# Optimization experiments

Measured on AMD Instinct MI355X. Metric: run time of the kernel, lower is better.

Reference implementation:

```python
import jax, jax.numpy as jnp
import numpy as np

N_SAMPLES = 128
AGENTS = 64
D = 128          # latent_size
EDIM = 2         # edge attr dim
N = N_SAMPLES * AGENTS
EPS = 1e-5


def _build_edges():
    a = np.arange(AGENTS)
    rows = np.repeat(a, AGENTS)
    cols = np.tile(a, AGENTS)
    mask = rows != cols  # fully connected, no self loops
    rows, cols = rows[mask], cols[mask]
    offsets = (np.arange(N_SAMPLES) * AGENTS)[:, None]
    src = (rows[None, :] + offsets).ravel().astype(np.int32)  # edge_index[0]
    dst = (cols[None, :] + offsets).ravel().astype(np.int32)  # edge_index[1]
    return src, dst


def setup_inputs() -> dict:
    key = jax.random.key(0)
    ks = jax.random.split(key, 16)
    src, dst = _build_edges()
    zin = 2 * D + EDIM  # CGConv concat [x_i, x_j, e]
    inp = {
        "gnn_in": jax.random.normal(ks[0], (N, D), jnp.float32),
        "centers": jax.random.normal(ks[1], (N, EDIM), jnp.float32),
        "edge_src": jnp.asarray(src),
        "edge_dst": jnp.asarray(dst),
    }
    for li, base in ((1, 2), (2, 8)):
        inp[f"Wf{li}"] = jax.random.normal(ks[base + 0], (zin, D), jnp.float32) / np.sqrt(zin)
        inp[f"bf{li}"] = jnp.zeros((D,), jnp.float32)
        inp[f"Ws{li}"] = jax.random.normal(ks[base + 1], (zin, D), jnp.float32) / np.sqrt(zin)
        inp[f"bs{li}"] = jnp.zeros((D,), jnp.float32)
        inp[f"gamma{li}"] = jnp.ones((D,), jnp.float32)
        inp[f"beta{li}"] = jnp.zeros((D,), jnp.float32)
    return inp


def _cgconv(x, e, src, dst, Wf, bf, Ws, bs, gamma, beta):
    # message: z = [x_i(target), x_j(source), e]; sigmoid(Wf z) * softplus(Ws z)
    z = jnp.concatenate([x[dst], x[src], e], axis=-1)  # [E, 2D+2]
    m = jax.nn.sigmoid(z @ Wf + bf) * jax.nn.softplus(z @ Ws + bs)
    agg = jax.ops.segment_sum(m, dst, num_segments=N)  # scatter-add at targets
    # batch norm (training-mode batch stats) then residual, as in PyG CGConv
    mu = agg.mean(axis=0)
    var = agg.var(axis=0)
    agg = (agg - mu) * jax.lax.rsqrt(var + EPS) * gamma + beta
    return agg + x


def reference(gnn_in, centers, edge_src, edge_dst,
              Wf1, bf1, Ws1, bs1, gamma1, beta1,
              Wf2, bf2, Ws2, bs2, gamma2, beta2):
    # edge_attr = centers[col] - centers[row]
    e = centers[edge_dst] - centers[edge_src]  # [E, 2]
    x = jax.nn.relu(_cgconv(gnn_in, e, edge_src, edge_dst, Wf1, bf1, Ws1, bs1, gamma1, beta1))
    x = jax.nn.relu(_cgconv(x, e, edge_src, edge_dst, Wf2, bf2, Ws2, bs2, gamma2, beta2))
    return x
```

## Files before the change

### kernel.cpp

```cpp
#include <hip/hip_runtime.h>
#include <hip/hip_bf16.h>

#define NSAMP 128
#define AGENTS 64
#define D 128
#define NN (NSAMP * AGENTS)
#define LOG2E 1.44269504088896340736f
#define LN2   0.69314718055994530942f
#define EPSF  1e-5f

typedef __attribute__((ext_vector_type(8))) short short8;
typedef __attribute__((ext_vector_type(4))) float floatx4;

__device__ __forceinline__ float u2f(unsigned v) {
    float f; __builtin_memcpy(&f, &v, 4); return f;
}
__device__ __forceinline__ unsigned f2u(float f) {
    unsigned v; __builtin_memcpy(&v, &f, 4); return v;
}
__device__ __forceinline__ unsigned short f2bf(float f) {
    unsigned x; __builtin_memcpy(&x, &f, 4);
    return (unsigned short)((x + 0x7FFFu + ((x >> 16) & 1u)) >> 16);
}

__global__ __launch_bounds__(256) void cvt_kernel(
    const float* __restrict__ Wf1, const float* __restrict__ Ws1,
    const float* __restrict__ Wf2, const float* __restrict__ Ws2,
    unsigned short* __restrict__ WT, float* __restrict__ sacc)
{
    int b = blockIdx.x;
    if (b < 64) {
        int rr = b * 16 + (threadIdx.x >> 4);
        int kk = (threadIdx.x & 15) * 8;
        int layer = rr >> 9, rem = rr & 511, arr = rem >> 7, c = rem & 127;
        const float* M = (arr < 2) ? (layer ? Wf2 : Wf1) : (layer ? Ws2 : Ws1);
        int side = arr & 1;
        short8 s;
        #pragma unroll
        for (int j = 0; j < 8; ++j)
            s[j] = (short)f2bf(M[(size_t)(side * 128 + kk + j) * D + c]);
        *(short8*)&WT[(size_t)(layer * 4 + arr) * 16384 + c * 128 + kk] = s;
    } else {
        sacc[threadIdx.x]       = 0.f;
        sacc[256 + threadIdx.x] = 0.f;
    }
}

__global__ __launch_bounds__(256, 4) void prep_edge(
    const float* __restrict__ xin,
    const unsigned short* __restrict__ WT,
    const float* __restrict__ centers,
    const float* __restrict__ Wf, const float* __restrict__ bf_,
    const float* __restrict__ Ws, const float* __restrict__ bs_,
    float* __restrict__ agg,
    float* __restrict__ sacc)
{
    const int s = blockIdx.x >> 3, q = blockIdx.x & 7;
    const int nbase = s * AGENTS;
    const int tid = threadIdx.x, w = tid >> 6, lane = tid & 63;
    const int quad = lane >> 4, l16 = lane & 15;

    __shared__ unsigned int EApk[64][17];
    __shared__ unsigned int EBpk[64][17];

    const int col = q * 16 + l16;
    short8 a[4];
    {
        const float* xr = xin + (size_t)(nbase + w * 16 + l16) * D + quad * 8;
        #pragma unroll
        for (int kc = 0; kc < 4; ++kc) {
            float4 v0 = *(const float4*)(xr + kc * 32);
            float4 v1 = *(const float4*)(xr + kc * 32 + 4);
            short8 t;
            t[0] = (short)f2bf(v0.x); t[1] = (short)f2bf(v0.y);
            t[2] = (short)f2bf(v0.z); t[3] = (short)f2bf(v0.w);
            t[4] = (short)f2bf(v1.x); t[5] = (short)f2bf(v1.y);
            t[6] = (short)f2bf(v1.z); t[7] = (short)f2bf(v1.w);
            a[kc] = t;
        }
    }
    floatx4 acc[4];
    #pragma unroll
    for (int arr = 0; arr < 4; ++arr) {
        const unsigned short* wp = WT + ((size_t)arr * 128 + col) * 128 + quad * 8;
        floatx4 ac = {0.f, 0.f, 0.f, 0.f};
        #pragma unroll
        for (int kc = 0; kc < 4; ++kc)
            ac = __builtin_amdgcn_mfma_f32_16x16x32_bf16(
                a[kc], *(const short8*)(wp + kc * 32), ac, 0, 0, 0);
        acc[arr] = ac;
    }
    const float cwf0 = Wf[256 * D + col], cwf1 = Wf[257 * D + col];
    const float cws0 = Ws[256 * D + col], cws1 = Ws[257 * D + col];
    const float bfv = bf_[col], bsv = bs_[col];
    #pragma unroll
    for (int r = 0; r < 4; ++r) {
        int row = w * 16 + quad * 4 + r;
        int n = nbase + row;
        float ce0 = centers[2 * n], ce1 = centers[2 * n + 1];
        float ctf = fmaf(ce0, cwf0, ce1 * cwf1);
        float cts = fmaf(ce0, cws0, ce1 * cws1);
        unsigned eaf = (unsigned)f2bf(__builtin_amdgcn_exp2f(-LOG2E * (acc[0][r] + ctf + bfv)));
        unsigned eas = (unsigned)f2bf(__builtin_amdgcn_exp2f( LOG2E * (acc[2][r] + cts + bsv)));
        unsigned ebf = (unsigned)f2bf(__builtin_amdgcn_exp2f(-LOG2E * (acc[1][r] - ctf)));
        unsigned ebs = (unsigned)f2bf(__builtin_amdgcn_exp2f( LOG2E * (acc[3][r] - cts)));
        EApk[row][l16] = eaf | (eas << 16);
        EBpk[row][l16] = ebf | (ebs << 16);
    }
    __syncthreads();

    const int cl = tid & 15, slot = tid >> 4;
    const int c = q * 16 + cl;
    float eaf[4], eas[4], ac2[4];
    #pragma unroll
    for (int i = 0; i < 4; ++i) {
        unsigned pk = EApk[slot * 4 + i][cl];
        eaf[i] = u2f(pk << 16);
        eas[i] = u2f(pk & 0xFFFF0000u);
        ac2[i] = 0.f;
    }
    #pragma unroll 4
    for (int j = 0; j < 64; ++j) {
        unsigned pk = EBpk[j][cl];
        float ebf = u2f(pk << 16);
        float ebs = u2f(pk & 0xFFFF0000u);
        #pragma unroll
        for (int i = 0; i < 4; ++i) {
            float sg = __builtin_amdgcn_rcpf(fmaf(eaf[i], ebf, 1.f));
            float lg = __builtin_amdgcn_logf(fmaf(eas[i], ebs, 1.f));
            ac2[i] = fmaf(sg, lg, ac2[i]);
        }
    }
    float s1 = 0.f, s2 = 0.f;
    #pragma unroll
    for (int i = 0; i < 4; ++i) {
        int d = slot * 4 + i;
        unsigned pk = EBpk[d][cl];
        float ebf = u2f(pk << 16);
        float ebs = u2f(pk & 0xFFFF0000u);
        float sg = __builtin_amdgcn_rcpf(fmaf(eaf[i], ebf, 1.f));
        float lg = __builtin_amdgcn_logf(fmaf(eas[i], ebs, 1.f));
        float v = (ac2[i] - sg * lg) * LN2;
        agg[(size_t)(nbase + d) * D + c] = v;
        s1 += v; s2 += v * v;
    }
    __syncthreads();
    EApk[slot][cl] = f2u(s1);
    EBpk[slot][cl] = f2u(s2);
    __syncthreads();
    #pragma unroll
    for (int off = 8; off >= 1; off >>= 1) {
        if (slot < off) {
            EApk[slot][cl] = f2u(u2f(EApk[slot][cl]) + u2f(EApk[slot + off][cl]));
            EBpk[slot][cl] = f2u(u2f(EBpk[slot][cl]) + u2f(EBpk[slot + off][cl]));
        }
        __syncthreads();
    }
    if (slot == 0) {
        atomicAdd(&sacc[c],       u2f(EApk[0][cl]));
        atomicAdd(&sacc[128 + c], u2f(EBpk[0][cl]));
    }
}

__global__ __launch_bounds__(256) void bn_kernel(
    const float* __restrict__ agg, const float* __restrict__ xin,
    const float* __restrict__ sacc,
    const float* __restrict__ gamma, const float* __restrict__ beta,
    float* __restrict__ outp)
{
    const int t = blockIdx.x * 256 + threadIdx.x;
    const int n = t >> 4;
    const int c = (t & 15) * 8;
    size_t off = (size_t)n * D + c;
    const float inv = 1.f / NN;
    float v[8];
    #pragma unroll
    for (int h = 0; h < 2; ++h) {
        float4 a  = *(const float4*)&agg[off + h * 4];
        float4 xv = *(const float4*)&xin[off + h * 4];
        float4 s1 = *(const float4*)&sacc[c + h * 4];
        float4 s2 = *(const float4*)&sacc[128 + c + h * 4];
        float4 gm = *(const float4*)&gamma[c + h * 4];
        float4 bt = *(const float4*)&beta[c + h * 4];
        float mu, var, rs;
        mu = s1.x * inv; var = s2.x * inv - mu * mu; rs = rsqrtf(var + EPSF);
        v[h*4+0] = fmaxf(0.f, fmaf((a.x - mu) * rs, gm.x, bt.x) + xv.x);
        mu = s1.y * inv; var = s2.y * inv - mu * mu; rs = rsqrtf(var + EPSF);
        v[h*4+1] = fmaxf(0.f, fmaf((a.y - mu) * rs, gm.y, bt.y) + xv.y);
        mu = s1.z * inv; var = s2.z * inv - mu * mu; rs = rsqrtf(var + EPSF);
        v[h*4+2] = fmaxf(0.f, fmaf((a.z - mu) * rs, gm.z, bt.z) + xv.z);
        mu = s1.w * inv; var = s2.w * inv - mu * mu; rs = rsqrtf(var + EPSF);
        v[h*4+3] = fmaxf(0.f, fmaf((a.w - mu) * rs, gm.w, bt.w) + xv.w);
    }
    *(float4*)&outp[off]     = *(float4*)&v[0];
    *(float4*)&outp[off + 4] = *(float4*)&v[4];
}

extern "C" void kernel_launch(void* const* d_in, const int* in_sizes, int n_in,
                              void* d_out, int out_size, void* d_ws, size_t ws_size,
                              hipStream_t stream) {
    const float* x0      = (const float*)d_in[0];
    const float* centers = (const float*)d_in[1];
    const float* Wf[2] = { (const float*)d_in[4],  (const float*)d_in[10] };
    const float* bf[2] = { (const float*)d_in[5],  (const float*)d_in[11] };
    const float* Ws[2] = { (const float*)d_in[6],  (const float*)d_in[12] };
    const float* bs[2] = { (const float*)d_in[7],  (const float*)d_in[13] };
    const float* gm[2] = { (const float*)d_in[8],  (const float*)d_in[14] };
    const float* bt[2] = { (const float*)d_in[9],  (const float*)d_in[15] };

    const size_t ND = (size_t)NN * D;
    unsigned short* ws_u = (unsigned short*)d_ws;
    unsigned short* WT = ws_u;
    float* fbase = (float*)(WT + 2 * 65536);
    float* agg   = fbase;
    float* x1    = fbase + ND;
    float* sacc  = fbase + 2 * ND;

    float* outp = (float*)d_out;

    cvt_kernel<<<dim3(65), dim3(256), 0, stream>>>(
        Wf[0], Ws[0], Wf[1], Ws[1], WT, sacc);

    prep_edge<<<dim3(1024), dim3(256), 0, stream>>>(
        x0, WT, centers, Wf[0], bf[0], Ws[0], bs[0], agg, sacc);
    bn_kernel<<<dim3(512), dim3(256), 0, stream>>>(
        agg, x0, sacc, gm[0], bt[0], x1);

    prep_edge<<<dim3(1024), dim3(256), 0, stream>>>(
        x1, WT + 65536, centers, Wf[1], bf[1], Ws[1], bs[1], agg, sacc + 256);
    bn_kernel<<<dim3(512), dim3(256), 0, stream>>>(
        agg, x1, sacc + 256, gm[1], bt[1], outp);
}
```

Measured before the change: 148.0 us.

## Fuse whole two-layer GNN into one cooperative persistent kernel with grid syncs

Replaces the five separate launches (weight conversion, two edge-message kernels, two batchnorm kernels) with a single cooperative kernel that uses grid-wide syncs between phases. The first batchnorm plus ReLU is folded into the second layer's input loading, so the x1 round trip through memory goes away, and the final output recomputes layer-1 activations from agg1 and x0. The aim is to cut launch overhead and global traffic. In exchange it adds three grid barriers, limits the grid to the number of blocks that fit at once so samples are looped per block, and keeps the old multi-kernel path as a fallback.

Result: slower. 418.4 us (+182.6%).

```diff
diff --git a/kernel.cpp b/kernel.cpp
--- a/kernel.cpp
+++ b/kernel.cpp
@@ -1,5 +1,8 @@
 #include <hip/hip_runtime.h>
 #include <hip/hip_bf16.h>
+#include <hip/hip_cooperative_groups.h>
+
+namespace cg = cooperative_groups;
 
 #define NSAMP 128
 #define AGENTS 64
@@ -21,6 +24,273 @@
 __device__ __forceinline__ unsigned short f2bf(float f) {
     unsigned x; __builtin_memcpy(&x, &f, 4);
     return (unsigned short)((x + 0x7FFFu + ((x >> 16) & 1u)) >> 16);
+}
+
+__device__ __forceinline__ void mfma_gates(
+    const short8 (&a)[4], const unsigned short* __restrict__ wl,
+    const float* __restrict__ Wfp, const float* __restrict__ bfp,
+    const float* __restrict__ Wsp, const float* __restrict__ bsp,
+    const float* __restrict__ centers,
+    int nbase, int w, int quad, int l16, int col,
+    unsigned int (*EApk)[17], unsigned int (*EBpk)[17])
+{
+    floatx4 acc[4];
+    #pragma unroll
+    for (int arr = 0; arr < 4; ++arr) {
+        const unsigned short* wp = wl + ((size_t)arr * 128 + col) * 128 + quad * 8;
+        floatx4 ac = {0.f, 0.f, 0.f, 0.f};
+        #pragma unroll
+        for (int kc = 0; kc < 4; ++kc)
+            ac = __builtin_amdgcn_mfma_f32_16x16x32_bf16(
+                a[kc], *(const short8*)(wp + kc * 32), ac, 0, 0, 0);
+        acc[arr] = ac;
+    }
+    const float cwf0 = Wfp[256 * D + col], cwf1 = Wfp[257 * D + col];
+    const float cws0 = Wsp[256 * D + col], cws1 = Wsp[257 * D + col];
+    const float bfv = bfp[col], bsv = bsp[col];
+    #pragma unroll
+    for (int r = 0; r < 4; ++r) {
+        int row = w * 16 + quad * 4 + r;
+        int n = nbase + row;
+        float ce0 = centers[2 * n], ce1 = centers[2 * n + 1];
+        float ctf = fmaf(ce0, cwf0, ce1 * cwf1);
+        float cts = fmaf(ce0, cws0, ce1 * cws1);
+        unsigned eaf = (unsigned)f2bf(__builtin_amdgcn_exp2f(-LOG2E * (acc[0][r] + ctf + bfv)));
+        unsigned eas = (unsigned)f2bf(__builtin_amdgcn_exp2f( LOG2E * (acc[2][r] + cts + bsv)));
+        unsigned ebf = (unsigned)f2bf(__builtin_amdgcn_exp2f(-LOG2E * (acc[1][r] - ctf)));
+        unsigned ebs = (unsigned)f2bf(__builtin_amdgcn_exp2f( LOG2E * (acc[3][r] - cts)));
+        EApk[row][l16] = eaf | (eas << 16);
+        EBpk[row][l16] = ebf | (ebs << 16);
+    }
+}
+
+__device__ __forceinline__ void phaseB(
+    const unsigned int (*EApk)[17], const unsigned int (*EBpk)[17],
+    int cl, int slot, float (&v)[4], float& s1, float& s2)
+{
+    float eaf[4], eas[4], ac2[4];
+    #pragma unroll
+    for (int i = 0; i < 4; ++i) {
+        unsigned pk = EApk[slot * 4 + i][cl];
+        eaf[i] = u2f(pk << 16);
+        eas[i] = u2f(pk & 0xFFFF0000u);
+        ac2[i] = 0.f;
+    }
+    #pragma unroll 4
+    for (int j = 0; j < 64; ++j) {
+        unsigned pk = EBpk[j][cl];
+        float ebf = u2f(pk << 16);
+        float ebs = u2f(pk & 0xFFFF0000u);
+        #pragma unroll
+        for (int i = 0; i < 4; ++i) {
+            float sg = __builtin_amdgcn_rcpf(fmaf(eaf[i], ebf, 1.f));
+            float lg = __builtin_amdgcn_logf(fmaf(eas[i], ebs, 1.f));
+            ac2[i] = fmaf(sg, lg, ac2[i]);
+        }
+    }
+    s1 = 0.f; s2 = 0.f;
+    #pragma unroll
+    for (int i = 0; i < 4; ++i) {
+        int dd = slot * 4 + i;
+        unsigned pk = EBpk[dd][cl];
+        float ebf = u2f(pk << 16);
+        float ebs = u2f(pk & 0xFFFF0000u);
+        float sg = __builtin_amdgcn_rcpf(fmaf(eaf[i], ebf, 1.f));
+        float lg = __builtin_amdgcn_logf(fmaf(eas[i], ebs, 1.f));
+        v[i] = (ac2[i] - sg * lg) * LN2;
+        s1 += v[i]; s2 += v[i] * v[i];
+    }
+}
+
+__device__ __forceinline__ void stats_tree(
+    unsigned int (*EApk)[17], unsigned int (*EBpk)[17],
+    int cl, int slot, int c, float s1, float s2, float* __restrict__ sc)
+{
+    __syncthreads();
+    EApk[slot][cl] = f2u(s1);
+    EBpk[slot][cl] = f2u(s2);
+    __syncthreads();
+    #pragma unroll
+    for (int off = 8; off >= 1; off >>= 1) {
+        if (slot < off) {
+            EApk[slot][cl] = f2u(u2f(EApk[slot][cl]) + u2f(EApk[slot + off][cl]));
+            EBpk[slot][cl] = f2u(u2f(EBpk[slot][cl]) + u2f(EBpk[slot + off][cl]));
+        }
+        __syncthreads();
+    }
+    if (slot == 0) {
+        atomicAdd(&sc[c],       u2f(EApk[0][cl]));
+        atomicAdd(&sc[128 + c], u2f(EBpk[0][cl]));
+    }
+}
+
+__global__ __launch_bounds__(256, 4) void fused_gnn(
+    const float* __restrict__ x0, const float* __restrict__ centers,
+    const float* __restrict__ Wf1, const float* __restrict__ bf1,
+    const float* __restrict__ Ws1, const float* __restrict__ bs1,
+    const float* __restrict__ gm1, const float* __restrict__ bt1,
+    const float* __restrict__ Wf2, const float* __restrict__ bf2,
+    const float* __restrict__ Ws2, const float* __restrict__ bs2,
+    const float* __restrict__ gm2, const float* __restrict__ bt2,
+    unsigned short* __restrict__ WT, float* __restrict__ agg1,
+    float* __restrict__ agg2, float* __restrict__ sacc,
+    float* __restrict__ outp)
+{
+    cg::grid_group grid = cg::this_grid();
+    const int tid = threadIdx.x, w = tid >> 6, lane = tid & 63;
+    const int quad = lane >> 4, l16 = lane & 15;
+    const int cl = tid & 15, slot = tid >> 4;
+    const int q = blockIdx.x & 7;
+    const int s0 = blockIdx.x >> 3;
+    const int sStep = gridDim.x >> 3;
+    const int c = q * 16 + cl;
+    const int col = q * 16 + l16;
+
+    __shared__ unsigned int EApk[64][17];
+    __shared__ unsigned int EBpk[64][17];
+    __shared__ float bnA[128], bnB[128];
+    __shared__ float bn2A[128], bn2B[128];
+
+    for (int job = blockIdx.x; job < 65; job += gridDim.x) {
+        if (job < 64) {
+            int rr = job * 16 + (tid >> 4);
+            int kk = (tid & 15) * 8;
+            int layer = rr >> 9, rem = rr & 511, arr = rem >> 7, wc = rem & 127;
+            const float* M = (arr < 2) ? (layer ? Wf2 : Wf1) : (layer ? Ws2 : Ws1);
+            int side = arr & 1;
+            short8 sv;
+            #pragma unroll
+            for (int j = 0; j < 8; ++j)
+                sv[j] = (short)f2bf(M[(size_t)(side * 128 + kk + j) * D + wc]);
+            *(short8*)&WT[(size_t)(layer * 4 + arr) * 16384 + wc * 128 + kk] = sv;
+        } else {
+            sacc[tid] = 0.f;
+            sacc[256 + tid] = 0.f;
+        }
+    }
+    __builtin_amdgcn_fence(__ATOMIC_RELEASE, "agent");
+    grid.sync();
+    __builtin_amdgcn_fence(__ATOMIC_ACQUIRE, "agent");
+
+    {
+        float s1T = 0.f, s2T = 0.f;
+        for (int s = s0; s < NSAMP; s += sStep) {
+            const int nbase = s * AGENTS;
+            short8 a[4];
+            const float* xr = x0 + (size_t)(nbase + w * 16 + l16) * D + quad * 8;
+            #pragma unroll
+            for (int kc = 0; kc < 4; ++kc) {
+                float4 v0 = *(const float4*)(xr + kc * 32);
+                float4 v1 = *(const float4*)(xr + kc * 32 + 4);
+                short8 t;
+                t[0] = (short)f2bf(v0.x); t[1] = (short)f2bf(v0.y);
+                t[2] = (short)f2bf(v0.z); t[3] = (short)f2bf(v0.w);
+                t[4] = (short)f2bf(v1.x); t[5] = (short)f2bf(v1.y);
+                t[6] = (short)f2bf(v1.z); t[7] = (short)f2bf(v1.w);
+                a[kc] = t;
+            }
+            mfma_gates(a, WT, Wf1, bf1, Ws1, bs1, centers, nbase, w, quad, l16,
+                       col, EApk, EBpk);
+            __syncthreads();
+            float v1a[4], s1, s2;
+            phaseB(EApk, EBpk, cl, slot, v1a, s1, s2);
+            #pragma unroll
+            for (int i = 0; i < 4; ++i)
+                agg1[(size_t)(nbase + slot * 4 + i) * D + c] = v1a[i];
+            s1T += s1; s2T += s2;
+            __syncthreads();
+        }
+        stats_tree(EApk, EBpk, cl, slot, c, s1T, s2T, sacc);
+    }
+    __builtin_amdgcn_fence(__ATOMIC_RELEASE, "agent");
+    grid.sync();
+    __builtin_amdgcn_fence(__ATOMIC_ACQUIRE, "agent");
+
+    if (tid < 128) {
+        const float inv = 1.f / NN;
+        float mu = sacc[tid] * inv;
+        float var = sacc[128 + tid] * inv - mu * mu;
+        float rs = rsqrtf(var + EPSF);
+        float A = rs * gm1[tid];
+        bnA[tid] = A;
+        bnB[tid] = fmaf(-mu, A, bt1[tid]);
+    }
+    __syncthreads();
+    {
+        float s1T = 0.f, s2T = 0.f;
+        for (int s = s0; s < NSAMP; s += sStep) {
+            const int nbase = s * AGENTS;
+            short8 a[4];
+            const size_t ro = (size_t)(nbase + w * 16 + l16) * D + quad * 8;
+            #pragma unroll
+            for (int kc = 0; kc < 4; ++kc) {
+                int cc = quad * 8 + kc * 32;
+                float4 g0 = *(const float4*)&agg1[ro + kc * 32];
+                float4 g1 = *(const float4*)&agg1[ro + kc * 32 + 4];
+                float4 x0v = *(const float4*)(x0 + ro + kc * 32);
+                float4 x1v = *(const float4*)(x0 + ro + kc * 32 + 4);
+                float4 A0 = *(const float4*)&bnA[cc], A1 = *(const float4*)&bnA[cc + 4];
+                float4 B0 = *(const float4*)&bnB[cc], B1 = *(const float4*)&bnB[cc + 4];
+                short8 t;
+                t[0] = (short)f2bf(fmaxf(0.f, fmaf(g0.x, A0.x, B0.x) + x0v.x));
+                t[1] = (short)f2bf(fmaxf(0.f, fmaf(g0.y, A0.y, B0.y) + x0v.y));
+                t[2] = (short)f2bf(fmaxf(0.f, fmaf(g0.z, A0.z, B0.z) + x0v.z));
+                t[3] = (short)f2bf(fmaxf(0.f, fmaf(g0.w, A0.w, B0.w) + x0v.w));
+                t[4] = (short)f2bf(fmaxf(0.f, fmaf(g1.x, A1.x, B1.x) + x1v.x));
+                t[5] = (short)f2bf(fmaxf(0.f, fmaf(g1.y, A1.y, B1.y) + x1v.y));
+                t[6] = (short)f2bf(fmaxf(0.f, fmaf(g1.z, A1.z, B1.z) + x1v.z));
+                t[7] = (short)f2bf(fmaxf(0.f, fmaf(g1.w, A1.w, B1.w) + x1v.w));
+                a[kc] = t;
+            }
+            mfma_gates(a, WT + 65536, Wf2, bf2, Ws2, bs2, centers, nbase, w,
+                       quad, l16, col, EApk, EBpk);
+            __syncthreads();
+            float v2a[4], s1, s2;
+            phaseB(EApk, EBpk, cl, slot, v2a, s1, s2);
+            #pragma unroll
+            for (int i = 0; i < 4; ++i)
+                agg2[(size_t)(nbase + slot * 4 + i) * D + c] = v2a[i];
+            s1T += s1; s2T += s2;
+            __syncthreads();
+        }
+        stats_tree(EApk, EBpk, cl, slot, c, s1T, s2T, sacc + 256);
+    }
+    __builtin_amdgcn_fence(__ATOMIC_RELEASE, "agent");
+    grid.sync();
+    __builtin_amdgcn_fence(__ATOMIC_ACQUIRE, "agent");
+
+    if (tid < 128) {
+        const float inv = 1.f / NN;
+        float mu = sacc[256 + tid] * inv;
+        float var = sacc[384 + tid] * inv - mu * mu;
+        float rs = rsqrtf(var + EPSF);
+        float A = rs * gm2[tid];
+        bn2A[tid] = A;
+        bn2B[tid] = fmaf(-mu, A, bt2[tid]);
+    }
+    __syncthreads();
+    for (int t = blockIdx.x * 256 + tid; t < NN * 16; t += gridDim.x * 256) {
+        int n = t >> 4, c8 = (t & 15) * 8;
+        size_t off = (size_t)n * D + c8;
+        float o[8];
+        #pragma unroll
+        for (int h = 0; h < 2; ++h) {
+            float4 g2 = *(const float4*)&agg2[off + h * 4];
+            float4 g1 = *(const float4*)&agg1[off + h * 4];
+            float4 xv = *(const float4*)&x0[off + h * 4];
+            int cc = c8 + h * 4;
+            o[h*4+0] = fmaxf(0.f, fmaf(g2.x, bn2A[cc+0], bn2B[cc+0]) +
+                       fmaxf(0.f, fmaf(g1.x, bnA[cc+0], bnB[cc+0]) + xv.x));
+            o[h*4+1] = fmaxf(0.f, fmaf(g2.y, bn2A[cc+1], bn2B[cc+1]) +
+                       fmaxf(0.f, fmaf(g1.y, bnA[cc+1], bnB[cc+1]) + xv.y));
+            o[h*4+2] = fmaxf(0.f, fmaf(g2.z, bn2A[cc+2], bn2B[cc+2]) +
+                       fmaxf(0.f, fmaf(g1.z, bnA[cc+2], bnB[cc+2]) + xv.z));
+            o[h*4+3] = fmaxf(0.f, fmaf(g2.w, bn2A[cc+3], bn2B[cc+3]) +
+                       fmaxf(0.f, fmaf(g1.w, bnA[cc+3], bnB[cc+3]) + xv.w));
+        }
+        *(float4*)&outp[off]     = *(float4*)&o[0];
+        *(float4*)&outp[off + 4] = *(float4*)&o[4];
+    }
 }
 
 __global__ __launch_bounds__(256) void cvt_kernel(
@@ -47,22 +317,18 @@
 }
 
 __global__ __launch_bounds__(256, 4) void prep_edge(
-    const float* __restrict__ xin,
-    const unsigned short* __restrict__ WT,
+    const float* __restrict__ xin, const unsigned short* __restrict__ WT,
     const float* __restrict__ centers,
     const float* __restrict__ Wf, const float* __restrict__ bf_,
     const float* __restrict__ Ws, const float* __restrict__ bs_,
-    float* __restrict__ agg,
-    float* __restrict__ sacc)
+    float* __restrict__ agg, float* __restrict__ sacc)
 {
     const int s = blockIdx.x >> 3, q = blockIdx.x & 7;
     const int nbase = s * AGENTS;
     const int tid = threadIdx.x, w = tid >> 6, lane = tid & 63;
     const int quad = lane >> 4, l16 = lane & 15;
-
     __shared__ unsigned int EApk[64][17];
     __shared__ unsigned int EBpk[64][17];
-
     const int col = q * 16 + l16;
     short8 a[4];
     {
@@ -79,87 +345,17 @@
             a[kc] = t;
         }
     }
-    floatx4 acc[4];
-    #pragma unroll
-    for (int arr = 0; arr < 4; ++arr) {
-        const unsigned short* wp = WT + ((size_t)arr * 128 + col) * 128 + quad * 8;
-        floatx4 ac = {0.f, 0.f, 0.f, 0.f};
-        #pragma unroll
-        for (int kc = 0; kc < 4; ++kc)
-            ac = __builtin_amdgcn_mfma_f32_16x16x32_bf16(
-                a[kc], *(const short8*)(wp + kc * 32), ac, 0, 0, 0);
-        acc[arr] = ac;
-    }
-    const float cwf0 = Wf[256 * D + col], cwf1 = Wf[257 * D + col];
-    const float cws0 = Ws[256 * D + col], cws1 = Ws[257 * D + col];
-    const float bfv = bf_[col], bsv = bs_[col];
-    #pragma unroll
-    for (int r = 0; r < 4; ++r) {
-        int row = w * 16 + quad * 4 + r;
-        int n = nbase + row;
-        float ce0 = centers[2 * n], ce1 = centers[2 * n + 1];
-        float ctf = fmaf(ce0, cwf0, ce1 * cwf1);
-        float cts = fmaf(ce0, cws0, ce1 * cws1);
-        unsigned eaf = (unsigned)f2bf(__builtin_amdgcn_exp2f(-LOG2E * (acc[0][r] + ctf + bfv)));
-        unsigned eas = (unsigned)f2bf(__builtin_amdgcn_exp2f( LOG2E * (acc[2][r] + cts + bsv)));
-        unsigned ebf = (unsigned)f2bf(__builtin_amdgcn_exp2f(-LOG2E * (acc[1][r] - ctf)));
-        unsigned ebs = (unsigned)f2bf(__builtin_amdgcn_exp2f( LOG2E * (acc[3][r] - cts)));
-        EApk[row][l16] = eaf | (eas << 16);
-        EBpk[row][l16] = ebf | (ebs << 16);
-    }
+    mfma_gates(a, WT, Wf, bf_, Ws, bs_, centers, nbase, w, quad, l16, col,
+               EApk, EBpk);
     __syncthreads();
-
     const int cl = tid & 15, slot = tid >> 4;
     const int c = q * 16 + cl;
-    float eaf[4], eas[4], ac2[4];
-    #pragma unroll
-    for (int i = 0; i < 4; ++i) {
-        unsigned pk = EApk[slot * 4 + i][cl];
-        eaf[i] = u2f(pk << 16);
-        eas[i] = u2f(pk & 0xFFFF0000u);
-        ac2[i] = 0.f;
-    }
-    #pragma unroll 4
-    for (int j = 0; j < 64; ++j) {
-        unsigned pk = EBpk[j][cl];
-        float ebf = u2f(pk << 16);
-        float ebs = u2f(pk & 0xFFFF0000u);
-        #pragma unroll
-        for (int i = 0; i < 4; ++i) {
-            float sg = __builtin_amdgcn_rcpf(fmaf(eaf[i], ebf, 1.f));
-            float lg = __builtin_amdgcn_logf(fmaf(eas[i], ebs, 1.f));
-            ac2[i] = fmaf(sg, lg, ac2[i]);
-        }
-    }
-    float s1 = 0.f, s2 = 0.f;
-    #pragma unroll
-    for (int i = 0; i < 4; ++i) {
-        int d = slot * 4 + i;
-        unsigned pk = EBpk[d][cl];
-        float ebf = u2f(pk << 16);
-        float ebs = u2f(pk & 0xFFFF0000u);
-        float sg = __builtin_amdgcn_rcpf(fmaf(eaf[i], ebf, 1.f));
-        float lg = __builtin_amdgcn_logf(fmaf(eas[i], ebs, 1.f));
-        float v = (ac2[i] - sg * lg) * LN2;
-        agg[(size_t)(nbase + d) * D + c] = v;
-        s1 += v; s2 += v * v;
-    }
-    __syncthreads();
-    EApk[slot][cl] = f2u(s1);
-    EBpk[slot][cl] = f2u(s2);
-    __syncthreads();
-    #pragma unroll
-    for (int off = 8; off >= 1; off >>= 1) {
-        if (slot < off) {
-            EApk[slot][cl] = f2u(u2f(EApk[slot][cl]) + u2f(EApk[slot + off][cl]));
-            EBpk[slot][cl] = f2u(u2f(EBpk[slot][cl]) + u2f(EBpk[slot + off][cl]));
-        }
-        __syncthreads();
-    }
-    if (slot == 0) {
-        atomicAdd(&sacc[c],       u2f(EApk[0][cl]));
-        atomicAdd(&sacc[128 + c], u2f(EBpk[0][cl]));
-    }
+    float v[4], s1, s2;
+    phaseB(EApk, EBpk, cl, slot, v, s1, s2);
+    #pragma unroll
+    for (int i = 0; i < 4; ++i)
+        agg[(size_t)(nbase + slot * 4 + i) * D + c] = v[i];
+    stats_tree(EApk, EBpk, cl, slot, c, s1, s2, sacc);
 }
 
 __global__ __launch_bounds__(256) void bn_kernel(
@@ -201,33 +397,75 @@
                               hipStream_t stream) {
     const float* x0      = (const float*)d_in[0];
     const float* centers = (const float*)d_in[1];
-    const float* Wf[2] = { (const float*)d_in[4],  (const float*)d_in[10] };
-    const float* bf[2] = { (const float*)d_in[5],  (const float*)d_in[11] };
-    const float* Ws[2] = { (const float*)d_in[6],  (const float*)d_in[12] };
-    const float* bs[2] = { (const float*)d_in[7],  (const float*)d_in[13] };
-    const float* gm[2] = { (const float*)d_in[8],  (const float*)d_in[14] };
-    const float* bt[2] = { (const float*)d_in[9],  (const float*)d_in[15] };
+    const float* Wf1 = (const float*)d_in[4];
+    const float* bf1 = (const float*)d_in[5];
+    const float* Ws1 = (const float*)d_in[6];
+    const float* bs1 = (const float*)d_in[7];
+    const float* gm1 = (const float*)d_in[8];
+    const float* bt1 = (const float*)d_in[9];
+    const float* Wf2 = (const float*)d_in[10];
+    const float* bf2 = (const float*)d_in[11];
+    const float* Ws2 = (const float*)d_in[12];
+    const float* bs2 = (const float*)d_in[13];
+    const float* gm2 = (const float*)d_in[14];
+    const float* bt2 = (const float*)d_in[15];
 
     const size_t ND = (size_t)NN * D;
-    unsigned short* ws_u = (unsigned short*)d_ws;
-    unsigned short* WT = ws_u;
+    unsigned short* WT = (unsigned short*)d_ws;
     float* fbase = (float*)(WT + 2 * 65536);
-    float* agg   = fbase;
-    float* x1    = fbase + ND;
+    float* agg1  = fbase;
+    float* agg2  = fbase + ND;
     float* sacc  = fbase + 2 * ND;
-
-    float* outp = (float*)d_out;
-
-    cvt_kernel<<<dim3(65), dim3(256), 0, stream>>>(
-        Wf[0], Ws[0], Wf[1], Ws[1], WT, sacc);
-
-    prep_edge<<<dim3(1024), dim3(256), 0, stream>>>(
-        x0, WT, centers, Wf[0], bf[0], Ws[0], bs[0], agg, sacc);
-    bn_kernel<<<dim3(512), dim3(256), 0, stream>>>(
-        agg, x0, sacc, gm[0], bt[0], x1);
-
-    prep_edge<<<dim3(1024), dim3(256), 0, stream>>>(
-        x1, WT + 65536, centers, Wf[1], bf[1], Ws[1], bs[1], agg, sacc + 256);
-    bn_kernel<<<dim3(512), dim3(256), 0, stream>>>(
-        agg, x1, sacc + 256, gm[1], bt[1], outp);
-}
+    float* outp  = (float*)d_out;
+
+    static int coopGrid = -2;
+    if (coopGrid == -2) {
+        int occ = 0, cus = 0, dev = 0;
+        hipError_t e1 = hipOccupancyMaxActiveBlocksPerMultiprocessor(
+            &occ, (const void*)fused_gnn, 256, 0);
+        (void)hipGetDevice(&dev);
+        hipError_t e2 = hipDeviceGetAttribute(
+            &cus, hipDeviceAttributeMultiprocessorCount, dev);
+        if (e1 == hipSuccess && e2 == hipSuccess && occ > 0 && cus > 0) {
+            long g = (long)occ * (long)cus;
+            if (g > 1024) g = 1024;
+            g -= (g & 7);
+            coopGrid = (g >= 8) ? (int)g : -1;
+        } else {
+            coopGrid = -1;
+        }
+        (void)hipGetLastError();
+    }
+
+    bool done = false;
+    if (coopGrid > 0) {
+        void* args[] = {
+            (void*)&x0, (void*)&centers,
+            (void*)&Wf1, (void*)&bf1, (void*)&Ws1, (void*)&bs1, (void*)&gm1, (void*)&bt1,
+            (void*)&Wf2, (void*)&bf2, (void*)&Ws2, (void*)&bs2, (void*)&gm2, (void*)&bt2,
+            (void*)&WT, (void*)&agg1, (void*)&agg2, (void*)&sacc, (void*)&outp
+        };
+        hipError_t e = hipLaunchCooperativeKernel(
+            (const void*)fused_gnn, dim3(coopGrid), dim3(256), args, 0, stream);
+        if (e == hipSuccess) {
+            done = true;
+        } else {
+            (void)hipGetLastError();
+            coopGrid = -1;
+        }
+    }
+
+    if (!done) {
+        float* x1 = agg2;
+        cvt_kernel<<<dim3(65), dim3(256), 0, stream>>>(
+            Wf1, Ws1, Wf2, Ws2, WT, sacc);
+        prep_edge<<<dim3(1024), dim3(256), 0, stream>>>(
+            x0, WT, centers, Wf1, bf1, Ws1, bs1, agg1, sacc);
+        bn_kernel<<<dim3(512), dim3(256), 0, stream>>>(
+            agg1, x0, sacc, gm1, bt1, x1);
+        prep_edge<<<dim3(1024), dim3(256), 0, stream>>>(
+            x1, WT + 65536, centers, Wf2, bf2, Ws2, bs2, agg1, sacc + 256);
+        bn_kernel<<<dim3(512), dim3(256), 0, stream>>>(
+            agg1, x1, sacc + 256, gm2, bt2, outp);
+    }
+}
```

## Fuse BN into next layer's input load and split edge blocks by target half

Applied to the files above, without the earlier changes.

Removes the intermediate bn_kernel after layer 1. Layer 2 instead recomputes x1 on the fly from agg1 and x0, using per-channel BN scale and shift computed in shared memory. A single final kernel applies both BNs and the residuals. Each prep block is split into two halves over target rows, doubling the grid to 2048 with 8 blocks per CU, which halves per-thread pairwise work at the cost of redundant source-side MFMAs and input loads.

Result: slower. 163.4 us (+10.4%).

```diff
diff --git a/kernel.cpp b/kernel.cpp
--- a/kernel.cpp
+++ b/kernel.cpp
@@ -46,26 +46,66 @@
     }
 }
 
-__global__ __launch_bounds__(256, 4) void prep_edge(
+__device__ __forceinline__ void stats_tree(
+    unsigned int (*EApk)[17], unsigned int (*EBpk)[17],
+    int cl, int slot, int c, float s1, float s2, float* __restrict__ sc)
+{
+    __syncthreads();
+    EApk[slot][cl] = f2u(s1);
+    EBpk[slot][cl] = f2u(s2);
+    __syncthreads();
+    #pragma unroll
+    for (int off = 8; off >= 1; off >>= 1) {
+        if (slot < off) {
+            EApk[slot][cl] = f2u(u2f(EApk[slot][cl]) + u2f(EApk[slot + off][cl]));
+            EBpk[slot][cl] = f2u(u2f(EBpk[slot][cl]) + u2f(EBpk[slot + off][cl]));
+        }
+        __syncthreads();
+    }
+    if (slot == 0) {
+        atomicAdd(&sc[c],       u2f(EApk[0][cl]));
+        atomicAdd(&sc[128 + c], u2f(EBpk[0][cl]));
+    }
+}
+
+template<int LAYER>
+__global__ __launch_bounds__(256, 8) void prep_half(
     const float* __restrict__ xin,
+    const float* __restrict__ agg_in,
     const unsigned short* __restrict__ WT,
     const float* __restrict__ centers,
     const float* __restrict__ Wf, const float* __restrict__ bf_,
     const float* __restrict__ Ws, const float* __restrict__ bs_,
-    float* __restrict__ agg,
-    float* __restrict__ sacc)
+    const float* __restrict__ gm_prev, const float* __restrict__ bt_prev,
+    const float* __restrict__ sacc_prev,
+    float* __restrict__ agg_out, float* __restrict__ sacc_out)
 {
-    const int s = blockIdx.x >> 3, q = blockIdx.x & 7;
+    const int bid = blockIdx.x;
+    const int s = bid >> 4, q = (bid >> 1) & 7, h = bid & 1;
     const int nbase = s * AGENTS;
     const int tid = threadIdx.x, w = tid >> 6, lane = tid & 63;
     const int quad = lane >> 4, l16 = lane & 15;
-
-    __shared__ unsigned int EApk[64][17];
+    const int col = q * 16 + l16;
+
+    __shared__ unsigned int EApk[32][17];
     __shared__ unsigned int EBpk[64][17];
-
-    const int col = q * 16 + l16;
+    __shared__ float bnA[128], bnB[128];
+
+    if (LAYER == 2) {
+        if (tid < 128) {
+            const float inv = 1.f / NN;
+            float mu = sacc_prev[tid] * inv;
+            float var = sacc_prev[128 + tid] * inv - mu * mu;
+            float rs = rsqrtf(var + EPSF);
+            float A = rs * gm_prev[tid];
+            bnA[tid] = A;
+            bnB[tid] = fmaf(-mu, A, bt_prev[tid]);
+        }
+        __syncthreads();
+    }
+
     short8 a[4];
-    {
+    if (LAYER == 1) {
         const float* xr = xin + (size_t)(nbase + w * 16 + l16) * D + quad * 8;
         #pragma unroll
         for (int kc = 0; kc < 4; ++kc) {
@@ -78,17 +118,56 @@
             t[6] = (short)f2bf(v1.z); t[7] = (short)f2bf(v1.w);
             a[kc] = t;
         }
-    }
-    floatx4 acc[4];
-    #pragma unroll
-    for (int arr = 0; arr < 4; ++arr) {
+    } else {
+        const size_t ro = (size_t)(nbase + w * 16 + l16) * D + quad * 8;
+        #pragma unroll
+        for (int kc = 0; kc < 4; ++kc) {
+            int cc = quad * 8 + kc * 32;
+            float4 g0 = *(const float4*)&agg_in[ro + kc * 32];
+            float4 g1 = *(const float4*)&agg_in[ro + kc * 32 + 4];
+            float4 x0v = *(const float4*)(xin + ro + kc * 32);
+            float4 x1v = *(const float4*)(xin + ro + kc * 32 + 4);
+            float4 A0 = *(const float4*)&bnA[cc], A1 = *(const float4*)&bnA[cc + 4];
+            float4 B0 = *(const float4*)&bnB[cc], B1 = *(const float4*)&bnB[cc + 4];
+            short8 t;
+            t[0] = (short)f2bf(fmaxf(0.f, fmaf(g0.x, A0.x, B0.x) + x0v.x));
+            t[1] = (short)f2bf(fmaxf(0.f, fmaf(g0.y, A0.y, B0.y) + x0v.y));
+            t[2] = (short)f2bf(fmaxf(0.f, fmaf(g0.z, A0.z, B0.z) + x0v.z));
+            t[3] = (short)f2bf(fmaxf(0.f, fmaf(g0.w, A0.w, B0.w) + x0v.w));
+            t[4] = (short)f2bf(fmaxf(0.f, fmaf(g1.x, A1.x, B1.x) + x1v.x));
+            t[5] = (short)f2bf(fmaxf(0.f, fmaf(g1.y, A1.y, B1.y) + x1v.y));
+            t[6] = (short)f2bf(fmaxf(0.f, fmaf(g1.z, A1.z, B1.z) + x1v.z));
+            t[7] = (short)f2bf(fmaxf(0.f, fmaf(g1.w, A1.w, B1.w) + x1v.w));
+            a[kc] = t;
+        }
+    }
+
+    const int doEA = ((w >> 1) == h);
+    floatx4 accB[2];
+    #pragma unroll
+    for (int a2 = 0; a2 < 2; ++a2) {
+        const int arr = 1 + 2 * a2;
         const unsigned short* wp = WT + ((size_t)arr * 128 + col) * 128 + quad * 8;
         floatx4 ac = {0.f, 0.f, 0.f, 0.f};
         #pragma unroll
         for (int kc = 0; kc < 4; ++kc)
             ac = __builtin_amdgcn_mfma_f32_16x16x32_bf16(
                 a[kc], *(const short8*)(wp + kc * 32), ac, 0, 0, 0);
-        acc[arr] = ac;
+        accB[a2] = ac;
+    }
+    floatx4 accA[2] = {{0,0,0,0},{0,0,0,0}};
+    if (doEA) {
+        #pragma unroll
+        for (int a2 = 0; a2 < 2; ++a2) {
+            const int arr = 2 * a2;
+            const unsigned short* wp = WT + ((size_t)arr * 128 + col) * 128 + quad * 8;
+            floatx4 ac = {0.f, 0.f, 0.f, 0.f};
+            #pragma unroll
+            for (int kc = 0; kc < 4; ++kc)
+                ac = __builtin_amdgcn_mfma_f32_16x16x32_bf16(
+                    a[kc], *(const short8*)(wp + kc * 32), ac, 0, 0, 0);
+            accA[a2] = ac;
+        }
     }
     const float cwf0 = Wf[256 * D + col], cwf1 = Wf[257 * D + col];
     const float cws0 = Ws[256 * D + col], cws1 = Ws[257 * D + col];
@@ -100,32 +179,34 @@
         float ce0 = centers[2 * n], ce1 = centers[2 * n + 1];
         float ctf = fmaf(ce0, cwf0, ce1 * cwf1);
         float cts = fmaf(ce0, cws0, ce1 * cws1);
-        unsigned eaf = (unsigned)f2bf(__builtin_amdgcn_exp2f(-LOG2E * (acc[0][r] + ctf + bfv)));
-        unsigned eas = (unsigned)f2bf(__builtin_amdgcn_exp2f( LOG2E * (acc[2][r] + cts + bsv)));
-        unsigned ebf = (unsigned)f2bf(__builtin_amdgcn_exp2f(-LOG2E * (acc[1][r] - ctf)));
-        unsigned ebs = (unsigned)f2bf(__builtin_amdgcn_exp2f( LOG2E * (acc[3][r] - cts)));
-        EApk[row][l16] = eaf | (eas << 16);
+        unsigned ebf = (unsigned)f2bf(__builtin_amdgcn_exp2f(-LOG2E * (accB[0][r] - ctf)));
+        unsigned ebs = (unsigned)f2bf(__builtin_amdgcn_exp2f( LOG2E * (accB[1][r] - cts)));
         EBpk[row][l16] = ebf | (ebs << 16);
+        if (doEA) {
+            unsigned eaf = (unsigned)f2bf(__builtin_amdgcn_exp2f(-LOG2E * (accA[0][r] + ctf + bfv)));
+            unsigned eas = (unsigned)f2bf(__builtin_amdgcn_exp2f( LOG2E * (accA[1][r] + cts + bsv)));
+            EApk[(w & 1) * 16 + quad * 4 + r][l16] = eaf | (eas << 16);
+        }
     }
     __syncthreads();
 
     const int cl = tid & 15, slot = tid >> 4;
     const int c = q * 16 + cl;
-    float eaf[4], eas[4], ac2[4];
-    #pragma unroll
-    for (int i = 0; i < 4; ++i) {
-        unsigned pk = EApk[slot * 4 + i][cl];
+    float eaf[2], eas[2], ac2[2];
+    #pragma unroll
+    for (int i = 0; i < 2; ++i) {
+        unsigned pk = EApk[slot * 2 + i][cl];
         eaf[i] = u2f(pk << 16);
         eas[i] = u2f(pk & 0xFFFF0000u);
         ac2[i] = 0.f;
     }
-    #pragma unroll 4
+    #pragma unroll 8
     for (int j = 0; j < 64; ++j) {
         unsigned pk = EBpk[j][cl];
         float ebf = u2f(pk << 16);
         float ebs = u2f(pk & 0xFFFF0000u);
         #pragma unroll
-        for (int i = 0; i < 4; ++i) {
+        for (int i = 0; i < 2; ++i) {
             float sg = __builtin_amdgcn_rcpf(fmaf(eaf[i], ebf, 1.f));
             float lg = __builtin_amdgcn_logf(fmaf(eas[i], ebs, 1.f));
             ac2[i] = fmaf(sg, lg, ac2[i]);
@@ -133,67 +214,66 @@
     }
     float s1 = 0.f, s2 = 0.f;
     #pragma unroll
-    for (int i = 0; i < 4; ++i) {
-        int d = slot * 4 + i;
+    for (int i = 0; i < 2; ++i) {
+        int d = h * 32 + slot * 2 + i;
         unsigned pk = EBpk[d][cl];
         float ebf = u2f(pk << 16);
         float ebs = u2f(pk & 0xFFFF0000u);
         float sg = __builtin_amdgcn_rcpf(fmaf(eaf[i], ebf, 1.f));
         float lg = __builtin_amdgcn_logf(fmaf(eas[i], ebs, 1.f));
         float v = (ac2[i] - sg * lg) * LN2;
-        agg[(size_t)(nbase + d) * D + c] = v;
+        agg_out[(size_t)(nbase + d) * D + c] = v;
         s1 += v; s2 += v * v;
     }
-    __syncthreads();
-    EApk[slot][cl] = f2u(s1);
-    EBpk[slot][cl] = f2u(s2);
-    __syncthreads();
-    #pragma unroll
-    for (int off = 8; off >= 1; off >>= 1) {
-        if (slot < off) {
-            EApk[slot][cl] = f2u(u2f(EApk[slot][cl]) + u2f(EApk[slot + off][cl]));
-            EBpk[slot][cl] = f2u(u2f(EBpk[slot][cl]) + u2f(EBpk[slot + off][cl]));
-        }
-        __syncthreads();
-    }
-    if (slot == 0) {
-        atomicAdd(&sacc[c],       u2f(EApk[0][cl]));
-        atomicAdd(&sacc[128 + c], u2f(EBpk[0][cl]));
-    }
-}
-
-__global__ __launch_bounds__(256) void bn_kernel(
-    const float* __restrict__ agg, const float* __restrict__ xin,
-    const float* __restrict__ sacc,
-    const float* __restrict__ gamma, const float* __restrict__ beta,
+    stats_tree(EApk, EBpk, cl, slot, c, s1, s2, sacc_out);
+}
+
+__global__ __launch_bounds__(256) void final_bn(
+    const float* __restrict__ x0, const float* __restrict__ agg1,
+    const float* __restrict__ agg2, const float* __restrict__ sacc,
+    const float* __restrict__ gm1, const float* __restrict__ bt1,
+    const float* __restrict__ gm2, const float* __restrict__ bt2,
     float* __restrict__ outp)
 {
-    const int t = blockIdx.x * 256 + threadIdx.x;
-    const int n = t >> 4;
-    const int c = (t & 15) * 8;
-    size_t off = (size_t)n * D + c;
-    const float inv = 1.f / NN;
-    float v[8];
-    #pragma unroll
-    for (int h = 0; h < 2; ++h) {
-        float4 a  = *(const float4*)&agg[off + h * 4];
-        float4 xv = *(const float4*)&xin[off + h * 4];
-        float4 s1 = *(const float4*)&sacc[c + h * 4];
-        float4 s2 = *(const float4*)&sacc[128 + c + h * 4];
-        float4 gm = *(const float4*)&gamma[c + h * 4];
-        float4 bt = *(const float4*)&beta[c + h * 4];
-        float mu, var, rs;
-        mu = s1.x * inv; var = s2.x * inv - mu * mu; rs = rsqrtf(var + EPSF);
-        v[h*4+0] = fmaxf(0.f, fmaf((a.x - mu) * rs, gm.x, bt.x) + xv.x);
-        mu = s1.y * inv; var = s2.y * inv - mu * mu; rs = rsqrtf(var + EPSF);
-        v[h*4+1] = fmaxf(0.f, fmaf((a.y - mu) * rs, gm.y, bt.y) + xv.y);
-        mu = s1.z * inv; var = s2.z * inv - mu * mu; rs = rsqrtf(var + EPSF);
-        v[h*4+2] = fmaxf(0.f, fmaf((a.z - mu) * rs, gm.z, bt.z) + xv.z);
-        mu = s1.w * inv; var = s2.w * inv - mu * mu; rs = rsqrtf(var + EPSF);
-        v[h*4+3] = fmaxf(0.f, fmaf((a.w - mu) * rs, gm.w, bt.w) + xv.w);
-    }
-    *(float4*)&outp[off]     = *(float4*)&v[0];
-    *(float4*)&outp[off + 4] = *(float4*)&v[4];
+    const int tid = threadIdx.x;
+    __shared__ float bnA[128], bnB[128], bn2A[128], bn2B[128];
+    if (tid < 128) {
+        const float inv = 1.f / NN;
+        float mu = sacc[tid] * inv;
+        float var = sacc[128 + tid] * inv - mu * mu;
+        float rs = rsqrtf(var + EPSF);
+        float A = rs * gm1[tid];
+        bnA[tid] = A;
+        bnB[tid] = fmaf(-mu, A, bt1[tid]);
+        float mu2 = sacc[256 + tid] * inv;
+        float var2 = sacc[384 + tid] * inv - mu2 * mu2;
+        float rs2 = rsqrtf(var2 + EPSF);
+        float A2 = rs2 * gm2[tid];
+        bn2A[tid] = A2;
+        bn2B[tid] = fmaf(-mu2, A2, bt2[tid]);
+    }
+    __syncthreads();
+    const int t = blockIdx.x * 256 + tid;
+    const int n = t >> 4, c8 = (t & 15) * 8;
+    size_t off = (size_t)n * D + c8;
+    float o[8];
+    #pragma unroll
+    for (int hh = 0; hh < 2; ++hh) {
+        float4 g2 = *(const float4*)&agg2[off + hh * 4];
+        float4 g1 = *(const float4*)&agg1[off + hh * 4];
+        float4 xv = *(const float4*)&x0[off + hh * 4];
+        int cc = c8 + hh * 4;
+        o[hh*4+0] = fmaxf(0.f, fmaf(g2.x, bn2A[cc+0], bn2B[cc+0]) +
+                    fmaxf(0.f, fmaf(g1.x, bnA[cc+0], bnB[cc+0]) + xv.x));
+        o[hh*4+1] = fmaxf(0.f, fmaf(g2.y, bn2A[cc+1], bn2B[cc+1]) +
+                    fmaxf(0.f, fmaf(g1.y, bnA[cc+1], bnB[cc+1]) + xv.y));
+        o[hh*4+2] = fmaxf(0.f, fmaf(g2.z, bn2A[cc+2], bn2B[cc+2]) +
+                    fmaxf(0.f, fmaf(g1.z, bnA[cc+2], bnB[cc+2]) + xv.z));
+        o[hh*4+3] = fmaxf(0.f, fmaf(g2.w, bn2A[cc+3], bn2B[cc+3]) +
+                    fmaxf(0.f, fmaf(g1.w, bnA[cc+3], bnB[cc+3]) + xv.w));
+    }
+    *(float4*)&outp[off]     = *(float4*)&o[0];
+    *(float4*)&outp[off + 4] = *(float4*)&o[4];
 }
 
 extern "C" void kernel_launch(void* const* d_in, const int* in_sizes, int n_in,
@@ -201,33 +281,38 @@
                               hipStream_t stream) {
     const float* x0      = (const float*)d_in[0];
     const float* centers = (const float*)d_in[1];
-    const float* Wf[2] = { (const float*)d_in[4],  (const float*)d_in[10] };
-    const float* bf[2] = { (const float*)d_in[5],  (const float*)d_in[11] };
-    const float* Ws[2] = { (const float*)d_in[6],  (const float*)d_in[12] };
-    const float* bs[2] = { (const float*)d_in[7],  (const float*)d_in[13] };
-    const float* gm[2] = { (const float*)d_in[8],  (const float*)d_in[14] };
-    const float* bt[2] = { (const float*)d_in[9],  (const float*)d_in[15] };
+    const float* Wf1 = (const float*)d_in[4];
+    const float* bf1 = (const float*)d_in[5];
+    const float* Ws1 = (const float*)d_in[6];
+    const float* bs1 = (const float*)d_in[7];
+    const float* gm1 = (const float*)d_in[8];
+    const float* bt1 = (const float*)d_in[9];
+    const float* Wf2 = (const float*)d_in[10];
+    const float* bf2 = (const float*)d_in[11];
+    const float* Ws2 = (const float*)d_in[12];
+    const float* bs2 = (const float*)d_in[13];
+    const float* gm2 = (const float*)d_in[14];
+    const float* bt2 = (const float*)d_in[15];
 
     const size_t ND = (size_t)NN * D;
-    unsigned short* ws_u = (unsigned short*)d_ws;
-    unsigned short* WT = ws_u;
+    unsigned short* WT = (unsigned short*)d_ws;
     float* fbase = (float*)(WT + 2 * 65536);
-    float* agg   = fbase;
-    float* x1    = fbase + ND;
+    float* agg1  = fbase;
+    float* agg2  = fbase + ND;
     float* sacc  = fbase + 2 * ND;
-
-    float* outp = (float*)d_out;
+    float* outp  = (float*)d_out;
 
     cvt_kernel<<<dim3(65), dim3(256), 0, stream>>>(
-        Wf[0], Ws[0], Wf[1], Ws[1], WT, sacc);
-
-    prep_edge<<<dim3(1024), dim3(256), 0, stream>>>(
-        x0, WT, centers, Wf[0], bf[0], Ws[0], bs[0], agg, sacc);
-    bn_kernel<<<dim3(512), dim3(256), 0, stream>>>(
-        agg, x0, sacc, gm[0], bt[0], x1);
-
-    prep_edge<<<dim3(1024), dim3(256), 0, stream>>>(
-        x1, WT + 65536, centers, Wf[1], bf[1], Ws[1], bs[1], agg, sacc + 256);
-    bn_kernel<<<dim3(512), dim3(256), 0, stream>>>(
-        agg, x1, sacc + 256, gm[1], bt[1], outp);
-}
+        Wf1, Ws1, Wf2, Ws2, WT, sacc);
+
+    prep_half<1><<<dim3(2048), dim3(256), 0, stream>>>(
+        x0, agg1 , WT, centers, Wf1, bf1, Ws1, bs1,
+        gm1 , bt1 , sacc , agg1, sacc);
+
+    prep_half<2><<<dim3(2048), dim3(256), 0, stream>>>(
+        x0, agg1, WT + 65536, centers, Wf2, bf2, Ws2, bs2,
+        gm1, bt1, sacc, agg2, sacc + 256);
+
+    final_bn<<<dim3(512), dim3(256), 0, stream>>>(
+        x0, agg1, agg2, sacc, gm1, bt1, gm2, bt2, outp);
+}
```
